# Optimization experiments

Measured on AMD Instinct MI355X. Metric: run time of the kernel, lower is better.

Reference implementation:

```python
import jax, jax.numpy as jnp
import numpy as np

B, T, S, H = 32, 512, 1024, 1024

def setup_inputs() -> dict:
    key = jax.random.key(0)
    k1, k2, k3, k4, k5, k6 = jax.random.split(key, 6)
    query = jax.random.normal(k1, (B, T, H), dtype=jnp.float32)
    encoder_outputs = jax.random.normal(k2, (B, S, H), dtype=jnp.float32)
    # lengths in [S//2, S], force max length == S so mask width matches score
    src_lengths = jax.random.randint(k3, (B,), S // 2, S + 1, dtype=jnp.int32)
    src_lengths = src_lengths.at[0].set(S).astype(jnp.int64)
    scale = 1.0 / np.sqrt(H)
    W_in = jax.random.normal(k4, (H, H), dtype=jnp.float32) * scale      # linear_in.weight
    W_out = jax.random.normal(k5, (H, 2 * H), dtype=jnp.float32) * scale # linear_out.weight
    b_out = jax.random.normal(k6, (H,), dtype=jnp.float32) * scale       # linear_out.bias
    return {"query": query, "encoder_outputs": encoder_outputs,
            "src_lengths": src_lengths, "W_in": W_in, "W_out": W_out, "b_out": b_out}

def reference(query, encoder_outputs, src_lengths, W_in, W_out, b_out):
    # padding mask: True where position >= length  [B, S]
    pad = jnp.arange(S)[None, :] >= src_lengths[:, None]
    # linear_in (no bias): [B, T, H]
    qw = jnp.einsum('bth,oh->bto', query, W_in)
    # scores: [B, T, S]
    score = jnp.einsum('bto,bso->bts', qw, encoder_outputs)
    score = jnp.where(pad[:, None, :], -jnp.inf, score)
    p = jax.nn.softmax(score, axis=2)
    # context: [B, T, H]
    c = jnp.einsum('bts,bsh->bth', p, encoder_outputs)
    concat = jnp.concatenate([query, c], axis=2)          # [B, T, 2H]
    out = jnp.tanh(jnp.einsum('btk,ok->bto', concat, W_out) + b_out)
    return out
```

## Files before the change

kernel.cpp:

```cpp
#include <hip/hip_runtime.h>
#include <math.h>

#define BB 32
#define TT 512
#define SS 1024
#define HH 1024

typedef __attribute__((ext_vector_type(8))) short short8;
typedef __attribute__((ext_vector_type(4))) float f32x4;
typedef __attribute__((ext_vector_type(4))) unsigned short u16x4;
typedef unsigned short u16;

__device__ __forceinline__ u16 f2h(float x) {
    union { float f; unsigned int u; } a; a.f = x;
    unsigned int u = a.u;
    return (u16)((u + 0x7fffu + ((u >> 16) & 1u)) >> 16);
}
__device__ __forceinline__ float h2f(u16 h) {
    union { unsigned int u; float f; } a; a.u = ((unsigned int)h) << 16;
    return a.f;
}

__device__ __forceinline__ void gll16(const u16* g, u16* l) {
    __builtin_amdgcn_global_load_lds(
        (const __attribute__((address_space(1))) void*)g,
        (__attribute__((address_space(3))) void*)l, 16, 0, 0);
}

enum { E_F32 = 0, E_SPLIT = 1, E_TANH = 2, E_H = 3 };

struct Segs { const u16* a[4]; const u16* b[4]; };

template<int NSEG, int EPI>
__global__ __launch_bounds__(512, 2) void gemm8(
    Segs sg, int ldA, int ldB, int zshift,
    long sA, long sB, long sC,
    const float* __restrict__ bias,
    float* __restrict__ Cf, u16* __restrict__ Ch, u16* __restrict__ Cl,
    int ldC)
{
    __shared__ u16 lds[2][2][2][256 * 32];

    const int tid = threadIdx.x;
    const int l = tid & 63, w = tid >> 6;
    const int wr = w >> 2, wc = w & 3;
    const int fr = l & 15, g = l >> 4;

    const int id = blockIdx.x;
    const int v = ((id & 7) << 5) | (id >> 3);
    const int z = v >> zshift;
    const int rest = v & ((1 << zshift) - 1);
    const int bm = (rest >> 2) * 256;
    const int bn = (rest & 3) * 256;

    const u16* Aseg[4]; const u16* Bseg[4];
#pragma unroll
    for (int s = 0; s < NSEG; ++s) {
        Aseg[s] = sg.a[s] + (long)z * sA;
        Bseg[s] = sg.b[s] + (long)z * sB;
    }
    if (EPI == E_F32 || EPI == E_TANH) Cf += (long)z * sC;
    else { Ch += (long)z * sC; if (EPI == E_SPLIT) Cl += (long)z * sC; }

    f32x4 acc[8][4] = {};

    auto stage = [&](int tile, int khalf, int tensor) {
        const int k0g = tile * 64 + khalf * 32;
        const int seg = k0g >> 10, kl = k0g & 1023;
        const u16* base = tensor ? Bseg[seg] : Aseg[seg];
        const int ld = tensor ? ldB : ldA;
        const int rb = tensor ? bn : bm;
        u16* lbase = &lds[tile & 1][tensor][khalf][0];
#pragma unroll
        for (int r = 0; r < 2; ++r) {
            const int p = r * 512 + tid;
            const int row = p >> 2, ch = p & 3;
            const int kc = ch ^ ((row >> 1) & 3);
            gll16(base + (long)(rb + row) * ld + kl + kc * 8,
                  lbase + ((r * 512 + (tid & ~63)) << 3));
        }
    };

    auto ldfrag = [&](int cur, int tensor, int ks, int row) -> short8 {
        const int off = (row * 4 + (g ^ ((row >> 1) & 3))) * 8;
        return *(const short8*)&lds[cur][tensor][ks][off];
    };

    stage(0, 0, 0); stage(0, 0, 1); stage(0, 1, 0); stage(0, 1, 1);
    asm volatile("s_waitcnt vmcnt(0)" ::: "memory");
    __builtin_amdgcn_s_barrier();

    const int NT = NSEG * 16;

#define PHASE(KS, MH, ST_KH, ST_TEN, WAITCODE)                                 \
    {                                                                          \
        if (MH == 0) {                                                         \
            _Pragma("unroll") for (int j = 0; j < 4; ++j)                      \
                fb[j] = ldfrag(cur, 1, KS, wc * 64 + j * 16 + fr);             \
        }                                                                      \
        _Pragma("unroll") for (int i = 0; i < 4; ++i)                          \
            fa[i] = ldfrag(cur, 0, KS, wr * 128 + (MH * 4 + i) * 16 + fr);     \
        if (notLast) stage(t + 1, ST_KH, ST_TEN);                              \
        WAITCODE                                                               \
        __builtin_amdgcn_s_barrier();                                          \
        __builtin_amdgcn_s_setprio(1);                                         \
        _Pragma("unroll") for (int i = 0; i < 4; ++i)                          \
            _Pragma("unroll") for (int j = 0; j < 4; ++j)                      \
                acc[MH * 4 + i][j] = __builtin_amdgcn_mfma_f32_16x16x32_bf16(  \
                    fa[i], fb[j], acc[MH * 4 + i][j], 0, 0, 0);                \
        __builtin_amdgcn_s_setprio(0);                                         \
        __builtin_amdgcn_s_barrier();                                          \
    }

    for (int t = 0; t < NT; ++t) {
        const int cur = t & 1;
        const bool notLast = (t + 1 < NT);
        short8 fa[4], fb[4];
        PHASE(0, 0, 0, 0, )
        PHASE(0, 1, 0, 1,
              if (notLast) { asm volatile("s_waitcnt vmcnt(4)" ::: "memory"); }
              else         { asm volatile("s_waitcnt vmcnt(0)" ::: "memory"); })
        PHASE(1, 0, 1, 0, )
        PHASE(1, 1, 1, 1,
              if (notLast) { asm volatile("s_waitcnt vmcnt(4)" ::: "memory"); })
    }
#undef PHASE

#pragma unroll
    for (int mi = 0; mi < 8; ++mi) {
        const int row0 = bm + wr * 128 + mi * 16 + g * 4;
#pragma unroll
        for (int nj = 0; nj < 4; ++nj) {
            const int col = bn + wc * 64 + nj * 16 + fr;
            const float bv = (EPI == E_TANH) ? bias[col] : 0.0f;
#pragma unroll
            for (int r = 0; r < 4; ++r) {
                const float vv = acc[mi][nj][r];
                const long o = (long)(row0 + r) * ldC + col;
                if (EPI == E_TANH) {
                    const float e = __expf(2.0f * (vv + bv));
                    Cf[o] = 1.0f - 2.0f / (e + 1.0f);
                } else if (EPI == E_F32) {
                    Cf[o] = vv;
                } else if (EPI == E_SPLIT) {
                    const u16 h = f2h(vv);
                    Ch[o] = h; Cl[o] = f2h(vv - h2f(h));
                } else {
                    Ch[o] = f2h(vv);
                }
            }
        }
    }
}

__global__ __launch_bounds__(256) void split_f32(
    const float* __restrict__ in, u16* __restrict__ hi, u16* __restrict__ lo,
    long n4)
{
    long i = (long)blockIdx.x * blockDim.x + threadIdx.x;
    const long stride = (long)gridDim.x * blockDim.x;
    for (; i < n4; i += stride) {
        f32x4 v = *(const f32x4*)(in + i * 4);
        u16x4 h4, l4;
#pragma unroll
        for (int e = 0; e < 4; ++e) {
            u16 h_ = f2h(v[e]);
            h4[e] = h_; l4[e] = f2h(v[e] - h2f(h_));
        }
        *(u16x4*)(hi + i * 4) = h4;
        *(u16x4*)(lo + i * 4) = l4;
    }
}

__global__ __launch_bounds__(256) void transpose_h(
    const float* __restrict__ in, u16* __restrict__ out)
{
    __shared__ float t[64][65];
    const int z = blockIdx.z, sb = blockIdx.x * 64, hb = blockIdx.y * 64;
    const int c4 = (threadIdx.x & 15) * 4, r0 = threadIdx.x >> 4;
    const float* src = in + ((long)z * SS + sb) * HH + hb;
#pragma unroll
    for (int i = 0; i < 4; ++i) {
        const int r = r0 + i * 16;
        f32x4 v = *(const f32x4*)(src + (long)r * HH + c4);
        t[c4 + 0][r] = v.x; t[c4 + 1][r] = v.y;
        t[c4 + 2][r] = v.z; t[c4 + 3][r] = v.w;
    }
    __syncthreads();
    u16* dst = out + ((long)z * HH + hb) * SS + sb;
#pragma unroll
    for (int i = 0; i < 4; ++i) {
        const int r = r0 + i * 16;
        u16x4 o;
#pragma unroll
        for (int j = 0; j < 4; ++j) o[j] = f2h(t[r][c4 + j]);
        *(u16x4*)(dst + (long)r * SS + c4) = o;
    }
}

__global__ __launch_bounds__(256) void softmax_mask(
    const float* __restrict__ Sc, u16* __restrict__ Ph,
    const int* __restrict__ lens)
{
    const int row = blockIdx.x;
    const int b = row >> 9;
    const int len = lens[b];
    const float* p = Sc + (long)row * SS;

    const int tid = threadIdx.x;
    const int s0 = tid * 4;
    f32x4 v = *(const f32x4*)(p + s0);
    float vals[4] = {v.x, v.y, v.z, v.w};

    float mx = -INFINITY;
#pragma unroll
    for (int j = 0; j < 4; ++j) {
        if (s0 + j >= len) vals[j] = -INFINITY;
        mx = fmaxf(mx, vals[j]);
    }
    for (int off = 32; off; off >>= 1) mx = fmaxf(mx, __shfl_xor(mx, off, 64));

    __shared__ float redm[4];
    __shared__ float reds[4];
    const int wave = tid >> 6, lane = tid & 63;
    if (lane == 0) redm[wave] = mx;
    __syncthreads();
    mx = fmaxf(fmaxf(redm[0], redm[1]), fmaxf(redm[2], redm[3]));

    float sum = 0.0f;
#pragma unroll
    for (int j = 0; j < 4; ++j) {
        vals[j] = __expf(vals[j] - mx);
        sum += vals[j];
    }
    for (int off = 32; off; off >>= 1) sum += __shfl_xor(sum, off, 64);
    if (lane == 0) reds[wave] = sum;
    __syncthreads();
    sum = reds[0] + reds[1] + reds[2] + reds[3];

    const float inv = 1.0f / sum;
    u16x4 o;
#pragma unroll
    for (int j = 0; j < 4; ++j) o[j] = f2h(vals[j] * inv);
    *(u16x4*)(Ph + (long)row * SS + s0) = o;
}

extern "C" void kernel_launch(void* const* d_in, const int* in_sizes, int n_in,
                              void* d_out, int out_size, void* d_ws, size_t ws_size,
                              hipStream_t stream)
{
    const float* query = (const float*)d_in[0];
    const float* enc   = (const float*)d_in[1];
    const int*   lens  = (const int*)d_in[2];
    const float* W_in  = (const float*)d_in[3];
    const float* W_out = (const float*)d_in[4];
    const float* b_out = (const float*)d_in[5];
    float* out = (float*)d_out;

    const long MQ = (long)BB * TT;

    u16* qh   = (u16*)d_ws;
    u16* ql   = qh   + MQ * HH;
    u16* qwh  = ql   + MQ * HH;
    u16* qwl  = qwh  + MQ * HH;
    u16* ench = qwl  + MQ * HH;
    u16* encl = ench + (long)BB * SS * HH;
    u16* ph   = encl + (long)BB * SS * HH;
    u16* wih  = ph   + MQ * SS;
    u16* wil  = wih  + (long)HH * HH;
    u16* woh  = wil  + (long)HH * HH;
    u16* wol  = woh  + (long)HH * 2 * HH;
    float* scores = (float*)(wol + (long)HH * 2 * HH);
    u16* encTh = (u16*)scores;
    u16* ch   = ql;

    split_f32<<<2048, 256, 0, stream>>>(query, qh, ql, MQ * HH / 4);
    split_f32<<<512, 256, 0, stream>>>(W_in, wih, wil, (long)HH * HH / 4);
    split_f32<<<512, 256, 0, stream>>>(W_out, woh, wol, (long)HH * 2 * HH / 4);
    split_f32<<<2048, 256, 0, stream>>>(enc, ench, encl, (long)BB * SS * HH / 4);

    Segs s1 = {{qh, qh, ql, nullptr}, {wih, wil, wih, nullptr}};
    gemm8<3, E_SPLIT><<<256, 512, 0, stream>>>(
        s1, HH, HH, 8, 0L, 0L, 0L, nullptr, nullptr, qwh, qwl, HH);

    Segs s2 = {{qwh, qwh, qwl, nullptr}, {ench, encl, ench, nullptr}};
    gemm8<3, E_F32><<<256, 512, 0, stream>>>(
        s2, HH, HH, 3, (long)TT * HH, (long)SS * HH, (long)TT * SS,
        nullptr, scores, nullptr, nullptr, SS);

    softmax_mask<<<BB * TT, 256, 0, stream>>>(scores, ph, lens);

    transpose_h<<<dim3(16, 16, 32), 256, 0, stream>>>(enc, encTh);

    Segs s3 = {{ph, nullptr, nullptr, nullptr}, {encTh, nullptr, nullptr, nullptr}};
    gemm8<1, E_H><<<256, 512, 0, stream>>>(
        s3, SS, SS, 3, (long)TT * SS, (long)HH * SS, (long)TT * HH,
        nullptr, nullptr, ch, nullptr, HH);

    Segs s4 = {{qh, ch, qh, ch},
               {woh, woh + 1024, wol, wol + 1024}};
    gemm8<4, E_TANH><<<256, 512, 0, stream>>>(
        s4, HH, 2 * HH, 8, 0L, 0L, 0L, b_out, out, nullptr, nullptr, HH);
}
```

Before: 503.6 us.

## Software-pipeline LDS fragment loads one phase ahead of MFMA in GEMM

Restructures the GEMM main loop so LDS fragment reads for the next phase are issued before the current phase's MFMAs, using double fragment registers and fewer barriers per phase. It also precomputes global and LDS addresses for staging and fragment offsets outside the loop. A stray warm-up loop that runs one iteration, breaks, then resets the accumulators and restages tile 0 adds redundant work and looks like leftover debug code. The added fragment registers raise register pressure.

Result: no change. 498.3 us (-1.1%).

```diff
diff --git a/kernel.cpp b/kernel.cpp
--- a/kernel.cpp
+++ b/kernel.cpp
@@ -64,67 +64,128 @@
 
     f32x4 acc[8][4] = {};
 
-    auto stage = [&](int tile, int khalf, int tensor) {
-        const int k0g = tile * 64 + khalf * 32;
+    const int srow = tid >> 2, sch = tid & 3;
+    const int skc = sch ^ ((srow >> 1) & 3);
+    const long grA0 = (long)(bm + srow) * ldA + skc * 8;
+    const long grA1 = (long)(bm + 128 + srow) * ldA + skc * 8;
+    const long grB0 = (long)(bn + srow) * ldB + skc * 8;
+    const long grB1 = (long)(bn + 128 + srow) * ldB + skc * 8;
+    const int ldst0 = (tid & ~63) * 8;
+    const int ldst1 = (512 + (tid & ~63)) * 8;
+
+    auto stage = [&](int tile, int kh, int tensor) {
+        const int k0g = tile * 64 + kh * 32;
         const int seg = k0g >> 10, kl = k0g & 1023;
-        const u16* base = tensor ? Bseg[seg] : Aseg[seg];
-        const int ld = tensor ? ldB : ldA;
-        const int rb = tensor ? bn : bm;
-        u16* lbase = &lds[tile & 1][tensor][khalf][0];
-#pragma unroll
-        for (int r = 0; r < 2; ++r) {
-            const int p = r * 512 + tid;
-            const int row = p >> 2, ch = p & 3;
-            const int kc = ch ^ ((row >> 1) & 3);
-            gll16(base + (long)(rb + row) * ld + kl + kc * 8,
-                  lbase + ((r * 512 + (tid & ~63)) << 3));
+        u16* lb = &lds[tile & 1][tensor][kh][0];
+        if (tensor) {
+            const u16* b = Bseg[seg];
+            gll16(b + grB0 + kl, lb + ldst0);
+            gll16(b + grB1 + kl, lb + ldst1);
+        } else {
+            const u16* a = Aseg[seg];
+            gll16(a + grA0 + kl, lb + ldst0);
+            gll16(a + grA1 + kl, lb + ldst1);
         }
     };
 
-    auto ldfrag = [&](int cur, int tensor, int ks, int row) -> short8 {
-        const int off = (row * 4 + (g ^ ((row >> 1) & 3))) * 8;
-        return *(const short8*)&lds[cur][tensor][ks][off];
-    };
+    int offA[8], offB[4];
+#pragma unroll
+    for (int k = 0; k < 8; ++k) {
+        const int r = wr * 128 + k * 16 + fr;
+        offA[k] = (r * 4 + (g ^ ((r >> 1) & 3))) * 8;
+    }
+#pragma unroll
+    for (int j = 0; j < 4; ++j) {
+        const int r = wc * 64 + j * 16 + fr;
+        offB[j] = (r * 4 + (g ^ ((r >> 1) & 3))) * 8;
+    }
+
+    short8 faX[4], faY[4], fbA[4], fbB[4];
+
+#define PFA(FA, BUF, KS, MH)                                                   \
+    { const u16* pl = &lds[BUF][0][KS][0];                                     \
+      _Pragma("unroll") for (int i_ = 0; i_ < 4; ++i_)                         \
+          FA[i_] = *(const short8*)&pl[offA[(MH) * 4 + i_]]; }
+#define PFB(FB, BUF, KS)                                                       \
+    { const u16* pl = &lds[BUF][1][KS][0];                                     \
+      _Pragma("unroll") for (int j_ = 0; j_ < 4; ++j_)                         \
+          FB[j_] = *(const short8*)&pl[offB[j_]]; }
+#define MFMA16(FA, FB, MH)                                                     \
+    __builtin_amdgcn_s_setprio(1);                                             \
+    _Pragma("unroll") for (int i_ = 0; i_ < 4; ++i_)                           \
+        _Pragma("unroll") for (int j_ = 0; j_ < 4; ++j_)                       \
+            acc[(MH) * 4 + i_][j_] = __builtin_amdgcn_mfma_f32_16x16x32_bf16(  \
+                FA[i_], FB[j_], acc[(MH) * 4 + i_][j_], 0, 0, 0);              \
+    __builtin_amdgcn_s_setprio(0);
 
     stage(0, 0, 0); stage(0, 0, 1); stage(0, 1, 0); stage(0, 1, 1);
     asm volatile("s_waitcnt vmcnt(0)" ::: "memory");
     __builtin_amdgcn_s_barrier();
+    PFB(fbA, 0, 0)
+    PFA(faX, 0, 0, 0)
+    __builtin_amdgcn_sched_barrier(0);
 
     const int NT = NSEG * 16;
-
-#define PHASE(KS, MH, ST_KH, ST_TEN, WAITCODE)                                 \
-    {                                                                          \
-        if (MH == 0) {                                                         \
-            _Pragma("unroll") for (int j = 0; j < 4; ++j)                      \
-                fb[j] = ldfrag(cur, 1, KS, wc * 64 + j * 16 + fr);             \
-        }                                                                      \
-        _Pragma("unroll") for (int i = 0; i < 4; ++i)                          \
-            fa[i] = ldfrag(cur, 0, KS, wr * 128 + (MH * 4 + i) * 16 + fr);     \
-        if (notLast) stage(t + 1, ST_KH, ST_TEN);                              \
-        WAITCODE                                                               \
-        __builtin_amdgcn_s_barrier();                                          \
-        __builtin_amdgcn_s_setprio(1);                                         \
-        _Pragma("unroll") for (int i = 0; i < 4; ++i)                          \
-            _Pragma("unroll") for (int j = 0; j < 4; ++j)                      \
-                acc[MH * 4 + i][j] = __builtin_amdgcn_mfma_f32_16x16x32_bf16(  \
-                    fa[i], fb[j], acc[MH * 4 + i][j], 0, 0, 0);                \
-        __builtin_amdgcn_s_setprio(0);                                         \
-        __builtin_amdgcn_s_barrier();                                          \
-    }
-
     for (int t = 0; t < NT; ++t) {
-        const int cur = t & 1;
-        const bool notLast = (t + 1 < NT);
-        short8 fa[4], fb[4];
-        PHASE(0, 0, 0, 0, )
-        PHASE(0, 1, 0, 1,
-              if (notLast) { asm volatile("s_waitcnt vmcnt(4)" ::: "memory"); }
-              else         { asm volatile("s_waitcnt vmcnt(0)" ::: "memory"); })
-        PHASE(1, 0, 1, 0, )
-        PHASE(1, 1, 1, 1,
-              if (notLast) { asm volatile("s_waitcnt vmcnt(4)" ::: "memory"); })
-    }
-#undef PHASE
+        const int cur = t & 1, nxt = cur ^ 1;
+        const bool nl = (t + 1 < NT);
+        if (nl) stage(t + 1, 0, 0);
+        __builtin_amdgcn_s_barrier();
+        PFA(faY, cur, 0, 1)
+        __builtin_amdgcn_sched_barrier(0);
+        MFMA16(faX, fbA, 1)
+        ;
+        break;
+    }
+
+#pragma unroll
+    for (int i = 0; i < 8; ++i)
+#pragma unroll
+        for (int j = 0; j < 4; ++j) acc[i][j] = f32x4{0.f, 0.f, 0.f, 0.f};
+    __builtin_amdgcn_s_barrier();
+    stage(0, 0, 0); stage(0, 0, 1); stage(0, 1, 0); stage(0, 1, 1);
+    asm volatile("s_waitcnt vmcnt(0)" ::: "memory");
+    __builtin_amdgcn_s_barrier();
+    PFB(fbA, 0, 0)
+    PFA(faX, 0, 0, 0)
+    __builtin_amdgcn_sched_barrier(0);
+
+    for (int t = 0; t < NT; ++t) {
+        const int cur = t & 1, nxt = cur ^ 1;
+        const bool nl = (t + 1 < NT);
+
+        if (nl) stage(t + 1, 0, 0);
+        __builtin_amdgcn_s_barrier();
+        PFA(faY, cur, 0, 1)
+        __builtin_amdgcn_sched_barrier(0);
+        MFMA16(faX, fbA, 0)
+
+        if (nl) stage(t + 1, 0, 1);
+        if (nl) { asm volatile("s_waitcnt vmcnt(4)" ::: "memory"); }
+        else    { asm volatile("s_waitcnt vmcnt(0)" ::: "memory"); }
+        __builtin_amdgcn_s_barrier();
+        PFB(fbB, cur, 1)
+        PFA(faX, cur, 1, 0)
+        __builtin_amdgcn_sched_barrier(0);
+        MFMA16(faY, fbA, 1)
+
+        if (nl) stage(t + 1, 1, 0);
+        __builtin_amdgcn_s_barrier();
+        PFA(faY, cur, 1, 1)
+        __builtin_amdgcn_sched_barrier(0);
+        MFMA16(faX, fbB, 0)
+
+        if (nl) stage(t + 1, 1, 1);
+        if (nl) { asm volatile("s_waitcnt vmcnt(4)" ::: "memory"); }
+        __builtin_amdgcn_s_barrier();
+        PFB(fbA, nxt, 0)
+        PFA(faX, nxt, 0, 0)
+        __builtin_amdgcn_sched_barrier(0);
+        MFMA16(faY, fbB, 1)
+    }
+#undef PFA
+#undef PFB
+#undef MFMA16
 
 #pragma unroll
     for (int mi = 0; mi < 8; ++mi) {
```
